# Optimization experiments

Hardware: AMD Instinct MI355X
Metric: run time of the kernel (lower is better)

The kernel has to match this reference:

```python
import jax, jax.numpy as jnp
import numpy as np

TOPK = 2  # matches init_kwargs topk


def setup_inputs() -> dict:
    key = jax.random.key(0)
    k1, k2 = jax.random.split(key)
    T, D, E = 32768, 4096, 16
    hidden_states = jax.random.normal(k1, (T, D), dtype=jnp.float32)
    wg_weight = jax.random.normal(k2, (E, D), dtype=jnp.float32) * 0.02  # [num_experts, hidden]
    return {"hidden_states": hidden_states, "wg_weight": wg_weight}


def reference(hidden_states, wg_weight):
    # logits = hidden_states @ wg.T  -> [T, E], computed in fp32 as in the torch module
    logits = jnp.einsum("td,ed->te", hidden_states.astype(jnp.float32), wg_weight.astype(jnp.float32))
    gates = jax.nn.softmax(logits, axis=-1)  # [T, E]
    topk_weights, topk_indices = jax.lax.top_k(gates, TOPK)  # [T, K] each
    topk_weights = topk_weights / jnp.sum(topk_weights, axis=-1, keepdims=True)
    return topk_indices, topk_weights.astype(hidden_states.dtype)
```

## Files before the change

### kernel.cpp

```cpp
#include <hip/hip_runtime.h>
#include <math.h>

#define T_TOKENS 32768
#define HID      4096
#define NEXP     16
#define MT       4
#define WAVES    4
#define D4       (HID / 4)
#define KI       (D4 / 64)

__global__ __launch_bounds__(256) void moe_gate_kernel(
    const float* __restrict__ h,
    const float* __restrict__ w,
    float* __restrict__ out)
{
    __shared__ float4 sw[2][NEXP][64];

    const int lane  = threadIdx.x & 63;
    const int wv    = threadIdx.x >> 6;
    const int t0    = (blockIdx.x * WAVES + wv) * MT;

    const float4* __restrict__ w4base = reinterpret_cast<const float4*>(w);
    const float4* hrow[MT];
    #pragma unroll
    for (int t = 0; t < MT; ++t)
        hrow[t] = reinterpret_cast<const float4*>(h + (size_t)(t0 + t) * HID);

    float acc[MT * NEXP];
    #pragma unroll
    for (int i = 0; i < MT * NEXP; ++i) acc[i] = 0.0f;

#define STAGE(b, ki) do {                                                     \
        _Pragma("unroll")                                                     \
        for (int j = 0; j < 4; ++j) {                                         \
            const int e = wv * 4 + j;                                         \
            const float4* gsrc = w4base + (size_t)e * D4 + (ki) * 64 + lane;  \
            __builtin_amdgcn_global_load_lds(                                 \
                (const __attribute__((address_space(1))) void*)gsrc,          \
                (__attribute__((address_space(3))) void*)&sw[b][e][0],        \
                16, 0, 0);                                                    \
        }                                                                     \
    } while (0)

    STAGE(0, 0);
    float4 hv[MT];
    #pragma unroll
    for (int t = 0; t < MT; ++t) hv[t] = hrow[t][lane];
    __syncthreads();

    int buf = 0;
    for (int ki = 0; ki < KI; ++ki) {
        float4 hn[MT];
        if (ki + 1 < KI) {
            STAGE(buf ^ 1, ki + 1);
            const int d4n = (ki + 1) * 64 + lane;
            #pragma unroll
            for (int t = 0; t < MT; ++t) hn[t] = hrow[t][d4n];
        }

        #pragma unroll
        for (int e = 0; e < NEXP; ++e) {
            float4 wvv = sw[buf][e][lane];
            #pragma unroll
            for (int t = 0; t < MT; ++t) {
                float a = acc[t * NEXP + e];
                a = fmaf(hv[t].x, wvv.x, a);
                a = fmaf(hv[t].y, wvv.y, a);
                a = fmaf(hv[t].z, wvv.z, a);
                a = fmaf(hv[t].w, wvv.w, a);
                acc[t * NEXP + e] = a;
            }
        }

        __syncthreads();
        buf ^= 1;
        #pragma unroll
        for (int t = 0; t < MT; ++t) hv[t] = hn[t];
    }

    #pragma unroll
    for (int b = 32; b >= 1; b >>= 1) {
        const bool hi = (lane & b) != 0;
        #pragma unroll
        for (int j = 0; j < b; ++j) {
            float lo_v = acc[j];
            float hi_v = acc[j + b];
            float keepv = hi ? hi_v : lo_v;
            float sendv = hi ? lo_v : hi_v;
            acc[j] = keepv + __shfl_xor(sendv, b, 64);
        }
    }
    const float logit = acc[0];

    const int eidx = lane & 15;
    float m1 = logit; int i1 = eidx;
    #pragma unroll
    for (int s = 1; s < 16; s <<= 1) {
        float ov = __shfl_xor(m1, s, 64);
        int   oi = __shfl_xor(i1, s, 64);
        if (ov > m1 || (ov == m1 && oi < i1)) { m1 = ov; i1 = oi; }
    }
    float masked = (eidx == i1) ? -INFINITY : logit;
    float m2 = masked; int i2 = eidx;
    #pragma unroll
    for (int s = 1; s < 16; s <<= 1) {
        float ov = __shfl_xor(m2, s, 64);
        int   oi = __shfl_xor(i2, s, 64);
        if (ov > m2 || (ov == m2 && oi < i2)) { m2 = ov; i2 = oi; }
    }

    if (eidx == 0) {
        const int t = t0 + (lane >> 4);
        const float r  = expf(m2 - m1);
        const float s  = 1.0f / (1.0f + r);
        float2* oidx = reinterpret_cast<float2*>(out);
        float2* owt  = reinterpret_cast<float2*>(out + 2 * T_TOKENS);
        oidx[t] = make_float2((float)i1, (float)i2);
        owt[t]  = make_float2(s, r * s);
    }
#undef STAGE
}

extern "C" void kernel_launch(void* const* d_in, const int* in_sizes, int n_in,
                              void* d_out, int out_size, void* d_ws, size_t ws_size,
                              hipStream_t stream) {
    const float* h = (const float*)d_in[0];
    const float* w = (const float*)d_in[1];
    float* out = (float*)d_out;

    const int blocks = T_TOKENS / (MT * WAVES);
    moe_gate_kernel<<<blocks, 256, 0, stream>>>(h, w, out);
}
```

Measured before the change: 122.2 us.

## Triple-buffer weight staging with explicit vmcnt waits and nontemporal hidden loads

Moves the gating GEMV from double to triple buffering of the weight tiles in LDS, prefetching two k-steps ahead for both weights and hidden-state registers. The full __syncthreads is replaced with partial s_waitcnt vmcnt counts plus s_barrier, so loads already in flight for later steps can keep running across the barrier. Hidden-state loads use nontemporal hints to avoid polluting cache with streaming data. This costs more LDS and registers, and the hand-counted vmcnt values must match the real number of outstanding loads or the results will be wrong.

```diff
diff --git a/kernel.cpp b/kernel.cpp
--- a/kernel.cpp
+++ b/kernel.cpp
@@ -9,74 +9,97 @@
 #define D4       (HID / 4)
 #define KI       (D4 / 64)
 
+typedef float f32x4 __attribute__((ext_vector_type(4)));
+
 __global__ __launch_bounds__(256) void moe_gate_kernel(
     const float* __restrict__ h,
     const float* __restrict__ w,
     float* __restrict__ out)
 {
-    __shared__ float4 sw[2][NEXP][64];
+    __shared__ f32x4 sw[3][NEXP][64];
 
-    const int lane  = threadIdx.x & 63;
-    const int wv    = threadIdx.x >> 6;
-    const int t0    = (blockIdx.x * WAVES + wv) * MT;
+    const int lane = threadIdx.x & 63;
+    const int wv   = threadIdx.x >> 6;
+    const int t0   = (blockIdx.x * WAVES + wv) * MT;
 
-    const float4* __restrict__ w4base = reinterpret_cast<const float4*>(w);
-    const float4* hrow[MT];
+    const f32x4* __restrict__ w4 = reinterpret_cast<const f32x4*>(w);
+    const f32x4* hrow[MT];
     #pragma unroll
     for (int t = 0; t < MT; ++t)
-        hrow[t] = reinterpret_cast<const float4*>(h + (size_t)(t0 + t) * HID);
+        hrow[t] = reinterpret_cast<const f32x4*>(h + (size_t)(t0 + t) * HID);
 
     float acc[MT * NEXP];
     #pragma unroll
     for (int i = 0; i < MT * NEXP; ++i) acc[i] = 0.0f;
 
-#define STAGE(b, ki) do {                                                     \
+#define STAGE(b, ki_) do {                                                    \
         _Pragma("unroll")                                                     \
         for (int j = 0; j < 4; ++j) {                                         \
-            const int e = wv * 4 + j;                                         \
-            const float4* gsrc = w4base + (size_t)e * D4 + (ki) * 64 + lane;  \
+            const int e_ = wv * 4 + j;                                        \
+            const f32x4* gsrc = w4 + (size_t)e_ * D4 + (ki_) * 64 + lane;     \
             __builtin_amdgcn_global_load_lds(                                 \
                 (const __attribute__((address_space(1))) void*)gsrc,          \
-                (__attribute__((address_space(3))) void*)&sw[b][e][0],        \
+                (__attribute__((address_space(3))) void*)&sw[b][e_][0],       \
                 16, 0, 0);                                                    \
         }                                                                     \
     } while (0)
 
+#define LOADH(dst, ki_) do {                                                  \
+        const int d4_ = (ki_) * 64 + lane;                                    \
+        _Pragma("unroll")                                                     \
+        for (int t = 0; t < MT; ++t)                                          \
+            dst[t] = __builtin_nontemporal_load(&hrow[t][d4_]);               \
+    } while (0)
+
+#define COMPUTE(b, hreg) do {                                                 \
+        _Pragma("unroll")                                                     \
+        for (int e_ = 0; e_ < NEXP; ++e_) {                                   \
+            f32x4 wvv = sw[b][e_][lane];                                      \
+            _Pragma("unroll")                                                 \
+            for (int t = 0; t < MT; ++t) {                                    \
+                float a = acc[t * NEXP + e_];                                 \
+                a = fmaf(hreg[t][0], wvv[0], a);                              \
+                a = fmaf(hreg[t][1], wvv[1], a);                              \
+                a = fmaf(hreg[t][2], wvv[2], a);                              \
+                a = fmaf(hreg[t][3], wvv[3], a);                              \
+                acc[t * NEXP + e_] = a;                                       \
+            }                                                                 \
+        }                                                                     \
+    } while (0)
+
+    f32x4 hv[MT], hn[MT];
     STAGE(0, 0);
-    float4 hv[MT];
-    #pragma unroll
-    for (int t = 0; t < MT; ++t) hv[t] = hrow[t][lane];
-    __syncthreads();
+    LOADH(hv, 0);
+    STAGE(1, 1);
+    LOADH(hn, 1);
+    asm volatile("s_waitcnt vmcnt(4)" ::: "memory");
+    __builtin_amdgcn_s_barrier();
+    asm volatile("" ::: "memory");
+    __builtin_amdgcn_sched_barrier(0);
 
-    int buf = 0;
-    for (int ki = 0; ki < KI; ++ki) {
-        float4 hn[MT];
-        if (ki + 1 < KI) {
-            STAGE(buf ^ 1, ki + 1);
-            const int d4n = (ki + 1) * 64 + lane;
-            #pragma unroll
-            for (int t = 0; t < MT; ++t) hn[t] = hrow[t][d4n];
-        }
+    int cur = 0;
+    for (int ki = 0; ki < KI - 2; ++ki) {
+        const int stg = (cur >= 1) ? cur - 1 : cur + 2;
+        STAGE(stg, ki + 2);
+        f32x4 h2[MT];
+        LOADH(h2, ki + 2);
+        COMPUTE(cur, hv);
+        #pragma unroll
+        for (int t = 0; t < MT; ++t) { hv[t] = hn[t]; hn[t] = h2[t]; }
+        asm volatile("s_waitcnt vmcnt(8)" ::: "memory");
+        __builtin_amdgcn_s_barrier();
+        asm volatile("" ::: "memory");
+        __builtin_amdgcn_sched_barrier(0);
+        cur = (cur >= 2) ? 0 : cur + 1;
+    }
 
-        #pragma unroll
-        for (int e = 0; e < NEXP; ++e) {
-            float4 wvv = sw[buf][e][lane];
-            #pragma unroll
-            for (int t = 0; t < MT; ++t) {
-                float a = acc[t * NEXP + e];
-                a = fmaf(hv[t].x, wvv.x, a);
-                a = fmaf(hv[t].y, wvv.y, a);
-                a = fmaf(hv[t].z, wvv.z, a);
-                a = fmaf(hv[t].w, wvv.w, a);
-                acc[t * NEXP + e] = a;
-            }
-        }
-
-        __syncthreads();
-        buf ^= 1;
-        #pragma unroll
-        for (int t = 0; t < MT; ++t) hv[t] = hn[t];
-    }
+    COMPUTE(cur, hv);
+    asm volatile("s_waitcnt vmcnt(0)" ::: "memory");
+    __builtin_amdgcn_s_barrier();
+    asm volatile("" ::: "memory");
+    __builtin_amdgcn_sched_barrier(0);
+    cur = (cur >= 2) ? 0 : cur + 1;
+    COMPUTE(cur, hn);
 
     #pragma unroll
     for (int b = 32; b >= 1; b >>= 1) {
@@ -119,6 +142,8 @@
         owt[t]  = make_float2(s, r * s);
     }
 #undef STAGE
+#undef LOADH
+#undef COMPUTE
 }
 
 extern "C" void kernel_launch(void* const* d_in, const int* in_sizes, int n_in,
```

New measurement: 118.0 us. -3.4%, faster.
